# Kernel optimization log

Measured on AMD Instinct MI355X. Metric: run time of the kernel, lower is better.

The kernel has to match this reference:

```python
import jax, jax.numpy as jnp
import numpy as np

T, B, IN = 216, 16384, 8
H1, H2 = 16, 64


def _lstm_scan(xs, h0, c0, Wih, Whh, bih, bhh):
    # xs: [T, B, D_in]; returns all hidden states [T, B, H]
    def step(carry, x_t):
        h, c = carry
        g = x_t @ Wih.T + bih + h @ Whh.T + bhh  # [B, 4H]
        i, f, gg, o = jnp.split(g, 4, axis=-1)
        c = jax.nn.sigmoid(f) * c + jax.nn.sigmoid(i) * jnp.tanh(gg)
        h = jax.nn.sigmoid(o) * jnp.tanh(c)
        return (h, c), h
    (_, _), hs = jax.lax.scan(step, (h0, c0), xs)
    return hs


def setup_inputs() -> dict:
    key = jax.random.key(0)
    ks = jax.random.split(key, 24)
    def rn(k, shape, std):
        return jax.random.normal(k, shape, dtype=jnp.float32) * std
    # PyTorch LSTMCell/Linear default init: U(-1/sqrt(H), 1/sqrt(H)) -> use uniform
    def un(k, shape, bound):
        return jax.random.uniform(k, shape, dtype=jnp.float32, minval=-bound, maxval=bound)
    b1 = 1.0 / np.sqrt(H1)
    b2 = 1.0 / np.sqrt(H2)
    inp = {
        'x': jax.random.normal(ks[0], (T, B, IN), dtype=jnp.float32),
        # initial states: kaiming_normal_ with fan_in = last dim -> std = sqrt(2/fan_in)
        'h0f': rn(ks[1], (B, H1), np.sqrt(2.0 / H1)),
        'c0f': rn(ks[2], (B, H1), np.sqrt(2.0 / H1)),
        'h0b': rn(ks[3], (B, H1), np.sqrt(2.0 / H1)),
        'c0b': rn(ks[4], (B, H1), np.sqrt(2.0 / H1)),
        'h0m': rn(ks[5], (B, H2), np.sqrt(2.0 / H2)),
        'c0m': rn(ks[6], (B, H2), np.sqrt(2.0 / H2)),
        'Wih_f': un(ks[7], (4 * H1, IN), b1), 'Whh_f': un(ks[8], (4 * H1, H1), b1),
        'bih_f': un(ks[9], (4 * H1,), b1), 'bhh_f': un(ks[10], (4 * H1,), b1),
        'Wih_b': un(ks[11], (4 * H1, IN), b1), 'Whh_b': un(ks[12], (4 * H1, H1), b1),
        'bih_b': un(ks[13], (4 * H1,), b1), 'bhh_b': un(ks[14], (4 * H1,), b1),
        'Wih_m': un(ks[15], (4 * H2, 2 * H1), b2), 'Whh_m': un(ks[16], (4 * H2, H2), b2),
        'bih_m': un(ks[17], (4 * H2,), b2), 'bhh_m': un(ks[18], (4 * H2,), b2),
        'Wd': un(ks[19], (1, H2), b2), 'bd': un(ks[20], (1,), b2),
    }
    return inp


def reference(x, h0f, c0f, h0b, c0b, h0m, c0m,
              Wih_f, Whh_f, bih_f, bhh_f,
              Wih_b, Whh_b, bih_b, bhh_b,
              Wih_m, Whh_m, bih_m, bhh_m,
              Wd, bd):
    # forward direction LSTM over time
    hs_f = _lstm_scan(x, h0f, c0f, Wih_f, Whh_f, bih_f, bhh_f)          # [T,B,16]
    # backward direction: run on reversed sequence, then reverse outputs
    hs_b = _lstm_scan(x[::-1], h0b, c0b, Wih_b, Whh_b, bih_b, bhh_b)[::-1]  # [T,B,16]
    mid_in = jnp.concatenate([hs_f, hs_b], axis=-1)                     # [T,B,32]
    hs_m = _lstm_scan(mid_in, h0m, c0m, Wih_m, Whh_m, bih_m, bhh_m)     # [T,B,64]
    # dropout is identity in inference reference; dense 64->1 per step
    out = jnp.einsum('tbh,oh->tbo', hs_m, Wd) + bd                      # [T,B,1]
    return out[:, :, 0].T                                                # [B,T]
```

## Files before the change

kernel.cpp:

```cpp
#include <hip/hip_runtime.h>

#define TT 216
#define BB 16384
#define LOG2E 1.44269504088896340736f

typedef _Float16 h16;
typedef _Float16 half8 __attribute__((ext_vector_type(8)));
typedef float f32x4 __attribute__((ext_vector_type(4)));

__device__ __forceinline__ float rcp_f(float v) { return __builtin_amdgcn_rcpf(v); }
__device__ __forceinline__ float ex2(float v)   { return __builtin_amdgcn_exp2f(v); }

__device__ __forceinline__ float lstm_up(float pi, float pf, float pg, float po, float& cs)
{
    float ei = ex2(pi), ef = ex2(pf), eg = ex2(pg), eo = ex2(po);
    float Ei = 1.f + ei, Ef = 1.f + ef, Eg = 1.f + eg, Eo = 1.f + eo;
    float EiEg = Ei * Eg;
    float G = fmaf(2.f * LOG2E, Eg, -4.f * LOG2E);
    float N = fmaf(cs, EiEg, Ef * G);
    cs = N * rcp_f(Ef * EiEg);
    float pc = fminf(cs, 60.f);
    float Ec = 1.f + ex2(pc);
    return (Ec - 2.f) * rcp_f(Eo * Ec);
}

__global__ void prep_kernel(
    const float* __restrict__ Wih_f, const float* __restrict__ Whh_f,
    const float* __restrict__ bih_f, const float* __restrict__ bhh_f,
    const float* __restrict__ Wih_b, const float* __restrict__ Whh_b,
    const float* __restrict__ bih_b, const float* __restrict__ bhh_b,
    const float* __restrict__ Wih_m, const float* __restrict__ Whh_m,
    const float* __restrict__ bih_m, const float* __restrict__ bhh_m,
    h16* __restrict__ W1f, h16* __restrict__ W1b, h16* __restrict__ W2)
{
    int gtid = blockIdx.x * blockDim.x + threadIdx.x;
    int gs = gridDim.x * blockDim.x;
    for (int idx = gtid; idx < 64 * 32; idx += gs) {
        int n = idx >> 5, k = idx & 31;
        float a = ((n >> 4) == 2) ? 2.f * LOG2E : -LOG2E;
        float vf = 0.f, vb = 0.f;
        if (k < 8)        { vf = Wih_f[n * 8 + k];       vb = Wih_b[n * 8 + k]; }
        else if (k < 24)  { vf = Whh_f[n * 16 + k - 8];  vb = Whh_b[n * 16 + k - 8]; }
        else if (k == 24) { vf = bih_f[n] + bhh_f[n];    vb = bih_b[n] + bhh_b[n]; }
        W1f[idx] = (h16)(vf * a);
        W1b[idx] = (h16)(vb * a);
    }
    for (int idx = gtid; idx < 256 * 128; idx += gs) {
        int n = idx >> 7, k = idx & 127;
        float a = ((n >> 6) == 2) ? 2.f * LOG2E : -LOG2E;
        float v = 0.f;
        if (k < 32)       v = Wih_m[n * 32 + k];
        else if (k < 96)  v = Whh_m[n * 64 + k - 32];
        else if (k == 96) v = bih_m[n] + bhh_m[n];
        W2[idx] = (h16)(v * a);
    }
}

__global__ __launch_bounds__(256, 2) void small_lstm_kernel(
    const float* __restrict__ x,
    const float* __restrict__ h0f, const float* __restrict__ c0f,
    const float* __restrict__ h0b, const float* __restrict__ c0b,
    const h16* __restrict__ W1f, const h16* __restrict__ W1b,
    h16* __restrict__ hsf, h16* __restrict__ hsb)
{
    __shared__ __attribute__((aligned(16))) h16 hbuf[4][16][24];

    const int tid = threadIdx.x;
    const int wv = tid >> 6, lane = tid & 63;
    const int b = lane & 15, q = lane >> 4;

    const int wgid = blockIdx.x * 4 + wv;
    const int dir  = wgid & 1;
    const int base = (wgid >> 1) * 16;

    const float* h0 = dir ? h0b : h0f;
    const float* c0 = dir ? c0b : c0f;
    const h16* W1   = dir ? W1b : W1f;
    h16* hs = dir ? hsb : hsf;

    half8 bf0 = *(const half8*)(W1 + (0 * 16 + b) * 32 + q * 8);
    half8 bf1 = *(const half8*)(W1 + (1 * 16 + b) * 32 + q * 8);
    half8 bf2 = *(const half8*)(W1 + (2 * 16 + b) * 32 + q * 8);
    half8 bf3 = *(const half8*)(W1 + (3 * 16 + b) * 32 + q * 8);

    float cs0 = c0[(size_t)(base + q * 4 + 0) * 16 + b] * (2.f * LOG2E);
    float cs1 = c0[(size_t)(base + q * 4 + 1) * 16 + b] * (2.f * LOG2E);
    float cs2 = c0[(size_t)(base + q * 4 + 2) * 16 + b] * (2.f * LOG2E);
    float cs3 = c0[(size_t)(base + q * 4 + 3) * 16 + b] * (2.f * LOG2E);

    const int t0 = dir ? (TT - 1) : 0;

    half8 af;
    if (q == 0) {
        const float* xp = x + ((size_t)t0 * BB + base + b) * 8;
        f32x4 u0 = *(const f32x4*)xp, u1 = *(const f32x4*)(xp + 4);
        af[0] = (h16)u0[0]; af[1] = (h16)u0[1]; af[2] = (h16)u0[2]; af[3] = (h16)u0[3];
        af[4] = (h16)u1[0]; af[5] = (h16)u1[1]; af[6] = (h16)u1[2]; af[7] = (h16)u1[3];
    } else if (q == 3) {
        af[0] = (h16)1.f;
        af[1] = (h16)0.f; af[2] = (h16)0.f; af[3] = (h16)0.f;
        af[4] = (h16)0.f; af[5] = (h16)0.f; af[6] = (h16)0.f; af[7] = (h16)0.f;
    } else {
        const float* hp = h0 + (size_t)(base + b) * 16 + (q - 1) * 8;
        f32x4 u0 = *(const f32x4*)hp, u1 = *(const f32x4*)(hp + 4);
        af[0] = (h16)u0[0]; af[1] = (h16)u0[1]; af[2] = (h16)u0[2]; af[3] = (h16)u0[3];
        af[4] = (h16)u1[0]; af[5] = (h16)u1[1]; af[6] = (h16)u1[2]; af[7] = (h16)u1[3];
    }

    f32x4 xr[4][2];
    if (q == 0) {
#pragma unroll
        for (int u = 1; u <= 3; ++u) {
            int tl = dir ? (TT - 1 - u) : u;
            const float* xp = x + ((size_t)tl * BB + base + b) * 8;
            xr[u][0] = *(const f32x4*)xp;
            xr[u][1] = *(const f32x4*)(xp + 4);
        }
    }

    for (int it = 0; it < TT / 4; ++it) {
        half8 hst[4];
#pragma unroll
        for (int j = 0; j < 4; ++j) {
            const int s = it * 4 + j;

            f32x4 z0 = {0.f, 0.f, 0.f, 0.f}, z1 = z0, z2 = z0, z3 = z0;
            z0 = __builtin_amdgcn_mfma_f32_16x16x32_f16(af, bf0, z0, 0, 0, 0);
            z1 = __builtin_amdgcn_mfma_f32_16x16x32_f16(af, bf1, z1, 0, 0, 0);
            z2 = __builtin_amdgcn_mfma_f32_16x16x32_f16(af, bf2, z2, 0, 0, 0);
            z3 = __builtin_amdgcn_mfma_f32_16x16x32_f16(af, bf3, z3, 0, 0, 0);

            half8 xh;
            {
                const f32x4 u0 = xr[(j + 1) & 3][0], u1 = xr[(j + 1) & 3][1];
                xh[0] = (h16)u0[0]; xh[1] = (h16)u0[1]; xh[2] = (h16)u0[2]; xh[3] = (h16)u0[3];
                xh[4] = (h16)u1[0]; xh[5] = (h16)u1[1]; xh[6] = (h16)u1[2]; xh[7] = (h16)u1[3];
            }
            if (q == 0) {
                int ut = (s + 4 < TT) ? (s + 4) : (TT - 1);
                int tl = dir ? (TT - 1 - ut) : ut;
                const float* xp = x + ((size_t)tl * BB + base + b) * 8;
                xr[j][0] = *(const f32x4*)xp;
                xr[j][1] = *(const f32x4*)(xp + 4);
            }

            float hh0 = lstm_up(z0[0], z1[0], z2[0], z3[0], cs0);
            float hh1 = lstm_up(z0[1], z1[1], z2[1], z3[1], cs1);
            float hh2 = lstm_up(z0[2], z1[2], z2[2], z3[2], cs2);
            float hh3 = lstm_up(z0[3], z1[3], z2[3], z3[3], cs3);

            hbuf[wv][q * 4 + 0][b] = (h16)hh0;
            hbuf[wv][q * 4 + 1][b] = (h16)hh1;
            hbuf[wv][q * 4 + 2][b] = (h16)hh2;
            hbuf[wv][q * 4 + 3][b] = (h16)hh3;
            asm volatile("s_waitcnt lgkmcnt(0)" ::: "memory");
            half8 hv = *(const half8*)&hbuf[wv][b][(q == 2) ? 8 : 0];
            hst[j] = hv;

            if (q == 0)      af = xh;
            else if (q != 3) af = hv;
        }
        if (q == 1 || q == 2) {
#pragma unroll
            for (int j = 0; j < 4; ++j) {
                int s = it * 4 + j;
                int t = dir ? (TT - 1 - s) : s;
                *(half8*)(hs + ((size_t)t * BB + base + b) * 16 + (q - 1) * 8) = hst[j];
            }
        }
    }
}

__global__ __launch_bounds__(256, 4) void mid_lstm_kernel(
    const h16* __restrict__ hsf, const h16* __restrict__ hsb,
    const float* __restrict__ h0m, const float* __restrict__ c0m,
    const h16* __restrict__ W2,
    const float* __restrict__ Wd, const float* __restrict__ bdp,
    float* __restrict__ out)
{
    __shared__ __attribute__((aligned(16))) h16 Xs[2][16][104];
    __shared__ float outbuf[16][55];

    const int tid = threadIdx.x;
    const int base = blockIdx.x * 16;
    const int wv = tid >> 6, lane = tid & 63, col = lane & 15, q = lane >> 4;

    half8 bfr[4][3];
    float bp[4];
#pragma unroll
    for (int p = 0; p < 4; ++p) {
        int n = p * 64 + wv * 16 + col;
#pragma unroll
        for (int kt = 0; kt < 3; ++kt)
            bfr[p][kt] = *(const half8*)(W2 + (size_t)n * 128 + kt * 32 + q * 8);
        bp[p] = (float)W2[(size_t)n * 128 + 96];
    }
    half8 dfr[2];
#pragma unroll
    for (int kt = 0; kt < 2; ++kt)
#pragma unroll
        for (int j = 0; j < 8; ++j)
            dfr[kt][j] = (col == 0) ? (h16)Wd[kt * 32 + q * 8 + j] : (h16)0.f;
    const float bdv = bdp[0];

    float cs[4];
#pragma unroll
    for (int r = 0; r < 4; ++r)
        cs[r] = c0m[(size_t)(base + q * 4 + r) * 64 + wv * 16 + col] * (2.f * LOG2E);

    const h16* hsrc = (wv == 1) ? hsb : hsf;
    const int srow = lane >> 1, su8 = (lane & 1) * 8;
    if (wv < 2 && lane < 32) {
        uint4 v = *(const uint4*)(hsrc + ((size_t)0 * BB + base + srow) * 16 + su8);
        *(uint4*)&Xs[0][srow][wv * 16 + su8] = v;
    }
    {
        int row = tid >> 4, u4 = (tid & 15) * 4;
        float4 v = *(const float4*)(h0m + (size_t)(base + row) * 64 + u4);
        h16* d = &Xs[0][row][32 + u4];
        d[0] = (h16)v.x; d[1] = (h16)v.y; d[2] = (h16)v.z; d[3] = (h16)v.w;
    }
    uint4 ra, rb;
    if (wv < 2 && lane < 32) {
        ra = *(const uint4*)(hsrc + ((size_t)1 * BB + base + srow) * 16 + su8);
        rb = *(const uint4*)(hsrc + ((size_t)2 * BB + base + srow) * 16 + su8);
    }
    __syncthreads();

    for (int t = 0; t < TT; ++t) {
        const int cur = t & 1, nxt = cur ^ 1;
        if (wv < 2 && lane < 32) {
            if (t < TT - 1)
                *(uint4*)&Xs[nxt][srow][wv * 16 + su8] = ra;
            ra = rb;
            int tl = (t + 3 < TT) ? (t + 3) : (TT - 1);
            rb = *(const uint4*)(hsrc + ((size_t)tl * BB + base + srow) * 16 + su8);
        }
        half8 af[3];
#pragma unroll
        for (int kt = 0; kt < 3; ++kt)
            af[kt] = *(const half8*)&Xs[cur][col][kt * 32 + q * 8];
        if (wv == 3 && t > 0) {
            f32x4 z = {0.f, 0.f, 0.f, 0.f};
            z = __builtin_amdgcn_mfma_f32_16x16x32_f16(af[1], dfr[0], z, 0, 0, 0);
            z = __builtin_amdgcn_mfma_f32_16x16x32_f16(af[2], dfr[1], z, 0, 0, 0);
            if (col == 0) {
                int tc = (t - 1) % 54;
#pragma unroll
                for (int r = 0; r < 4; ++r)
                    outbuf[q * 4 + r][tc] = z[r] + bdv;
            }
        }
        f32x4 acc[4];
        __builtin_amdgcn_s_setprio(1);
#pragma unroll
        for (int p = 0; p < 4; ++p) {
            f32x4 z = {bp[p], bp[p], bp[p], bp[p]};
            z = __builtin_amdgcn_mfma_f32_16x16x32_f16(af[0], bfr[p][0], z, 0, 0, 0);
            z = __builtin_amdgcn_mfma_f32_16x16x32_f16(af[1], bfr[p][1], z, 0, 0, 0);
            z = __builtin_amdgcn_mfma_f32_16x16x32_f16(af[2], bfr[p][2], z, 0, 0, 0);
            acc[p] = z;
        }
        __builtin_amdgcn_s_setprio(0);
#pragma unroll
        for (int r = 0; r < 4; ++r) {
            float h = lstm_up(acc[0][r], acc[1][r], acc[2][r], acc[3][r], cs[r]);
            Xs[nxt][q * 4 + r][32 + wv * 16 + col] = (h16)h;
        }
        if (t > 0 && (t % 54) == 0) {
            __syncthreads();
            int off = t - 54;
            for (int idx = tid; idx < 16 * 54; idx += 256) {
                int row = idx / 54, cc = idx - row * 54;
                out[(size_t)(base + row) * TT + off + cc] = outbuf[row][cc];
            }
        }
        __syncthreads();
    }
    if (wv == 3) {
        half8 a1 = *(const half8*)&Xs[0][col][32 + q * 8];
        half8 a2 = *(const half8*)&Xs[0][col][64 + q * 8];
        f32x4 z = {0.f, 0.f, 0.f, 0.f};
        z = __builtin_amdgcn_mfma_f32_16x16x32_f16(a1, dfr[0], z, 0, 0, 0);
        z = __builtin_amdgcn_mfma_f32_16x16x32_f16(a2, dfr[1], z, 0, 0, 0);
        if (col == 0)
#pragma unroll
            for (int r = 0; r < 4; ++r)
                outbuf[q * 4 + r][53] = z[r] + bdv;
    }
    __syncthreads();
    for (int idx = tid; idx < 16 * 54; idx += 256) {
        int row = idx / 54, cc = idx - row * 54;
        out[(size_t)(base + row) * TT + 162 + cc] = outbuf[row][cc];
    }
}

extern "C" void kernel_launch(void* const* d_in, const int* in_sizes, int n_in,
                              void* d_out, int out_size, void* d_ws, size_t ws_size,
                              hipStream_t stream)
{
    const float* x     = (const float*)d_in[0];
    const float* h0f   = (const float*)d_in[1];
    const float* c0f   = (const float*)d_in[2];
    const float* h0b   = (const float*)d_in[3];
    const float* c0b   = (const float*)d_in[4];
    const float* h0m   = (const float*)d_in[5];
    const float* c0m   = (const float*)d_in[6];
    const float* Wih_f = (const float*)d_in[7];
    const float* Whh_f = (const float*)d_in[8];
    const float* bih_f = (const float*)d_in[9];
    const float* bhh_f = (const float*)d_in[10];
    const float* Wih_b = (const float*)d_in[11];
    const float* Whh_b = (const float*)d_in[12];
    const float* bih_b = (const float*)d_in[13];
    const float* bhh_b = (const float*)d_in[14];
    const float* Wih_m = (const float*)d_in[15];
    const float* Whh_m = (const float*)d_in[16];
    const float* bih_m = (const float*)d_in[17];
    const float* bhh_m = (const float*)d_in[18];
    const float* Wd    = (const float*)d_in[19];
    const float* bd    = (const float*)d_in[20];

    char* ws = (char*)d_ws;
    h16* W1f = (h16*)(ws + 0);
    h16* W1b = (h16*)(ws + 4096);
    h16* W2  = (h16*)(ws + 8192);
    h16* hsf = (h16*)(ws + 73728);
    h16* hsb = (h16*)(ws + 73728 + (size_t)TT * BB * 16 * 2);

    prep_kernel<<<64, 256, 0, stream>>>(Wih_f, Whh_f, bih_f, bhh_f,
                                        Wih_b, Whh_b, bih_b, bhh_b,
                                        Wih_m, Whh_m, bih_m, bhh_m,
                                        W1f, W1b, W2);
    small_lstm_kernel<<<512, 256, 0, stream>>>(x, h0f, c0f, h0b, c0b,
                                               W1f, W1b, hsf, hsb);
    mid_lstm_kernel<<<1024, 256, 0, stream>>>(hsf, hsb, h0m, c0m, W2,
                                              Wd, bd, (float*)d_out);
}
```

Measured before the change: 648.5 us.

## Process two independent 16-row batch tiles per block in mid LSTM kernel

The mid LSTM kernel now has each block handle 32 batch rows as two independent 16-row windows, so the grid is halved. Each wave interleaves two MFMA chains and two gate-update passes, which adds independent work to hide the latency of the serial recurrence. The per-step barrier and the recurrent weight fragments are now shared across twice the rows, and the input-staging and dense-output work is spread over more waves. In exchange register pressure roughly doubles, launch bounds drop to 2 blocks per CU, and the setprio hints are removed, so occupancy falls.

```diff
diff --git a/kernel.cpp b/kernel.cpp
--- a/kernel.cpp
+++ b/kernel.cpp
@@ -171,18 +171,18 @@
     }
 }
 
-__global__ __launch_bounds__(256, 4) void mid_lstm_kernel(
+__global__ __launch_bounds__(256, 2) void mid_lstm_kernel(
     const h16* __restrict__ hsf, const h16* __restrict__ hsb,
     const float* __restrict__ h0m, const float* __restrict__ c0m,
     const h16* __restrict__ W2,
     const float* __restrict__ Wd, const float* __restrict__ bdp,
     float* __restrict__ out)
 {
-    __shared__ __attribute__((aligned(16))) h16 Xs[2][16][104];
-    __shared__ float outbuf[16][55];
+    __shared__ __attribute__((aligned(16))) h16 Xs[2][2][16][104];
+    __shared__ float outbuf[2][16][55];
 
     const int tid = threadIdx.x;
-    const int base = blockIdx.x * 16;
+    const int base = blockIdx.x * 32;
     const int wv = tid >> 6, lane = tid & 63, col = lane & 15, q = lane >> 4;
 
     half8 bfr[4][3];
@@ -203,95 +203,122 @@
             dfr[kt][j] = (col == 0) ? (h16)Wd[kt * 32 + q * 8 + j] : (h16)0.f;
     const float bdv = bdp[0];
 
-    float cs[4];
-#pragma unroll
-    for (int r = 0; r < 4; ++r)
-        cs[r] = c0m[(size_t)(base + q * 4 + r) * 64 + wv * 16 + col] * (2.f * LOG2E);
-
-    const h16* hsrc = (wv == 1) ? hsb : hsf;
+    float csA[4], csB[4];
+#pragma unroll
+    for (int r = 0; r < 4; ++r) {
+        csA[r] = c0m[(size_t)(base + q * 4 + r) * 64 + wv * 16 + col] * (2.f * LOG2E);
+        csB[r] = c0m[(size_t)(base + 16 + q * 4 + r) * 64 + wv * 16 + col] * (2.f * LOG2E);
+    }
+
+    const h16* hsrc = (wv & 1) ? hsb : hsf;
+    const int mywin = wv >> 1;
     const int srow = lane >> 1, su8 = (lane & 1) * 8;
-    if (wv < 2 && lane < 32) {
-        uint4 v = *(const uint4*)(hsrc + ((size_t)0 * BB + base + srow) * 16 + su8);
-        *(uint4*)&Xs[0][srow][wv * 16 + su8] = v;
+    const int scol = (wv & 1) * 16 + su8;
+    const int grow = base + mywin * 16 + srow;
+
+    if (lane < 32) {
+        uint4 v = *(const uint4*)(hsrc + ((size_t)0 * BB + grow) * 16 + su8);
+        *(uint4*)&Xs[mywin][0][srow][scol] = v;
     }
     {
         int row = tid >> 4, u4 = (tid & 15) * 4;
-        float4 v = *(const float4*)(h0m + (size_t)(base + row) * 64 + u4);
-        h16* d = &Xs[0][row][32 + u4];
-        d[0] = (h16)v.x; d[1] = (h16)v.y; d[2] = (h16)v.z; d[3] = (h16)v.w;
+        float4 vA = *(const float4*)(h0m + (size_t)(base + row) * 64 + u4);
+        h16* dA = &Xs[0][0][row][32 + u4];
+        dA[0] = (h16)vA.x; dA[1] = (h16)vA.y; dA[2] = (h16)vA.z; dA[3] = (h16)vA.w;
+        float4 vB = *(const float4*)(h0m + (size_t)(base + 16 + row) * 64 + u4);
+        h16* dB = &Xs[1][0][row][32 + u4];
+        dB[0] = (h16)vB.x; dB[1] = (h16)vB.y; dB[2] = (h16)vB.z; dB[3] = (h16)vB.w;
     }
     uint4 ra, rb;
-    if (wv < 2 && lane < 32) {
-        ra = *(const uint4*)(hsrc + ((size_t)1 * BB + base + srow) * 16 + su8);
-        rb = *(const uint4*)(hsrc + ((size_t)2 * BB + base + srow) * 16 + su8);
+    if (lane < 32) {
+        ra = *(const uint4*)(hsrc + ((size_t)1 * BB + grow) * 16 + su8);
+        rb = *(const uint4*)(hsrc + ((size_t)2 * BB + grow) * 16 + su8);
     }
     __syncthreads();
 
     for (int t = 0; t < TT; ++t) {
         const int cur = t & 1, nxt = cur ^ 1;
-        if (wv < 2 && lane < 32) {
+        if (lane < 32) {
             if (t < TT - 1)
-                *(uint4*)&Xs[nxt][srow][wv * 16 + su8] = ra;
+                *(uint4*)&Xs[mywin][nxt][srow][scol] = ra;
             ra = rb;
             int tl = (t + 3 < TT) ? (t + 3) : (TT - 1);
-            rb = *(const uint4*)(hsrc + ((size_t)tl * BB + base + srow) * 16 + su8);
-        }
-        half8 af[3];
-#pragma unroll
-        for (int kt = 0; kt < 3; ++kt)
-            af[kt] = *(const half8*)&Xs[cur][col][kt * 32 + q * 8];
-        if (wv == 3 && t > 0) {
+            rb = *(const uint4*)(hsrc + ((size_t)tl * BB + grow) * 16 + su8);
+        }
+        half8 afA[3], afB[3];
+#pragma unroll
+        for (int kt = 0; kt < 3; ++kt) {
+            afA[kt] = *(const half8*)&Xs[0][cur][col][kt * 32 + q * 8];
+            afB[kt] = *(const half8*)&Xs[1][cur][col][kt * 32 + q * 8];
+        }
+        if ((wv & 1) && t > 0) {
+            half8 a1 = (wv == 1) ? afA[1] : afB[1];
+            half8 a2 = (wv == 1) ? afA[2] : afB[2];
             f32x4 z = {0.f, 0.f, 0.f, 0.f};
-            z = __builtin_amdgcn_mfma_f32_16x16x32_f16(af[1], dfr[0], z, 0, 0, 0);
-            z = __builtin_amdgcn_mfma_f32_16x16x32_f16(af[2], dfr[1], z, 0, 0, 0);
+            z = __builtin_amdgcn_mfma_f32_16x16x32_f16(a1, dfr[0], z, 0, 0, 0);
+            z = __builtin_amdgcn_mfma_f32_16x16x32_f16(a2, dfr[1], z, 0, 0, 0);
             if (col == 0) {
                 int tc = (t - 1) % 54;
 #pragma unroll
                 for (int r = 0; r < 4; ++r)
-                    outbuf[q * 4 + r][tc] = z[r] + bdv;
-            }
-        }
-        f32x4 acc[4];
-        __builtin_amdgcn_s_setprio(1);
+                    outbuf[wv >> 1][q * 4 + r][tc] = z[r] + bdv;
+            }
+        }
+        f32x4 accA[4], accB[4];
 #pragma unroll
         for (int p = 0; p < 4; ++p) {
             f32x4 z = {bp[p], bp[p], bp[p], bp[p]};
-            z = __builtin_amdgcn_mfma_f32_16x16x32_f16(af[0], bfr[p][0], z, 0, 0, 0);
-            z = __builtin_amdgcn_mfma_f32_16x16x32_f16(af[1], bfr[p][1], z, 0, 0, 0);
-            z = __builtin_amdgcn_mfma_f32_16x16x32_f16(af[2], bfr[p][2], z, 0, 0, 0);
-            acc[p] = z;
-        }
-        __builtin_amdgcn_s_setprio(0);
+            z = __builtin_amdgcn_mfma_f32_16x16x32_f16(afA[0], bfr[p][0], z, 0, 0, 0);
+            z = __builtin_amdgcn_mfma_f32_16x16x32_f16(afA[1], bfr[p][1], z, 0, 0, 0);
+            z = __builtin_amdgcn_mfma_f32_16x16x32_f16(afA[2], bfr[p][2], z, 0, 0, 0);
+            accA[p] = z;
+        }
+#pragma unroll
+        for (int p = 0; p < 4; ++p) {
+            f32x4 z = {bp[p], bp[p], bp[p], bp[p]};
+            z = __builtin_amdgcn_mfma_f32_16x16x32_f16(afB[0], bfr[p][0], z, 0, 0, 0);
+            z = __builtin_amdgcn_mfma_f32_16x16x32_f16(afB[1], bfr[p][1], z, 0, 0, 0);
+            z = __builtin_amdgcn_mfma_f32_16x16x32_f16(afB[2], bfr[p][2], z, 0, 0, 0);
+            accB[p] = z;
+        }
 #pragma unroll
         for (int r = 0; r < 4; ++r) {
-            float h = lstm_up(acc[0][r], acc[1][r], acc[2][r], acc[3][r], cs[r]);
-            Xs[nxt][q * 4 + r][32 + wv * 16 + col] = (h16)h;
+            float hA = lstm_up(accA[0][r], accA[1][r], accA[2][r], accA[3][r], csA[r]);
+            Xs[0][nxt][q * 4 + r][32 + wv * 16 + col] = (h16)hA;
+        }
+#pragma unroll
+        for (int r = 0; r < 4; ++r) {
+            float hB = lstm_up(accB[0][r], accB[1][r], accB[2][r], accB[3][r], csB[r]);
+            Xs[1][nxt][q * 4 + r][32 + wv * 16 + col] = (h16)hB;
         }
         if (t > 0 && (t % 54) == 0) {
             __syncthreads();
             int off = t - 54;
-            for (int idx = tid; idx < 16 * 54; idx += 256) {
-                int row = idx / 54, cc = idx - row * 54;
-                out[(size_t)(base + row) * TT + off + cc] = outbuf[row][cc];
+            for (int idx = tid; idx < 2 * 16 * 54; idx += 256) {
+                int w = idx / (16 * 54), rem = idx - w * 16 * 54;
+                int row = rem / 54, cc = rem - row * 54;
+                out[(size_t)(base + w * 16 + row) * TT + off + cc] = outbuf[w][row][cc];
             }
         }
         __syncthreads();
     }
-    if (wv == 3) {
-        half8 a1 = *(const half8*)&Xs[0][col][32 + q * 8];
-        half8 a2 = *(const half8*)&Xs[0][col][64 + q * 8];
+    if (wv & 1) {
+        const int w = wv >> 1;
+        half8 a1 = *(const half8*)&Xs[w][0][col][32 + q * 8];
+        half8 a2 = *(const half8*)&Xs[w][0][col][64 + q * 8];
         f32x4 z = {0.f, 0.f, 0.f, 0.f};
         z = __builtin_amdgcn_mfma_f32_16x16x32_f16(a1, dfr[0], z, 0, 0, 0);
         z = __builtin_amdgcn_mfma_f32_16x16x32_f16(a2, dfr[1], z, 0, 0, 0);
         if (col == 0)
 #pragma unroll
             for (int r = 0; r < 4; ++r)
-                outbuf[q * 4 + r][53] = z[r] + bdv;
+                outbuf[w][q * 4 + r][53] = z[r] + bdv;
     }
     __syncthreads();
-    for (int idx = tid; idx < 16 * 54; idx += 256) {
-        int row = idx / 54, cc = idx - row * 54;
-        out[(size_t)(base + row) * TT + 162 + cc] = outbuf[row][cc];
+    for (int idx = tid; idx < 2 * 16 * 54; idx += 256) {
+        int w = idx / (16 * 54), rem = idx - w * 16 * 54;
+        int row = rem / 54, cc = rem - row * 54;
+        out[(size_t)(base + w * 16 + row) * TT + 162 + cc] = outbuf[w][row][cc];
     }
 }
 
@@ -334,6 +361,6 @@
                                         W1f, W1b, W2);
     small_lstm_kernel<<<512, 256, 0, stream>>>(x, h0f, c0f, h0b, c0b,
                                                W1f, W1b, hsf, hsb);
-    mid_lstm_kernel<<<1024, 256, 0, stream>>>(hsf, hsb, h0m, c0m, W2,
-                                              Wd, bd, (float*)d_out);
-}
+    mid_lstm_kernel<<<512, 256, 0, stream>>>(hsf, hsb, h0m, c0m, W2,
+                                             Wd, bd, (float*)d_out);
+}
```

Measured after the change: 680.4 us. 4.9% more time.

## Transpose small-LSTM MFMA to keep hidden state in registers via ds_swizzle

Applied to the files above, without the earlier changes.

The small bidirectional LSTM kernel now swaps the MFMA operands so each lane's output holds four consecutive hidden units of one batch row. The hidden state is then passed on with a ds_swizzle exchange between lane groups instead of a round trip through shared memory and a wait. Hidden states are written straight to global memory each step as 8-byte stores instead of batched 16-byte stores. The mid kernel's s_setprio hints around its MFMA block are also removed. This targets per-step LDS latency on the serial recurrence, at the cost of smaller, more frequent global stores.

```diff
diff --git a/kernel.cpp b/kernel.cpp
--- a/kernel.cpp
+++ b/kernel.cpp
@@ -6,7 +6,10 @@
 
 typedef _Float16 h16;
 typedef _Float16 half8 __attribute__((ext_vector_type(8)));
+typedef _Float16 h4 __attribute__((ext_vector_type(4)));
 typedef float f32x4 __attribute__((ext_vector_type(4)));
+typedef int i2 __attribute__((ext_vector_type(2)));
+typedef int i4 __attribute__((ext_vector_type(4)));
 
 __device__ __forceinline__ float rcp_f(float v) { return __builtin_amdgcn_rcpf(v); }
 __device__ __forceinline__ float ex2(float v)   { return __builtin_amdgcn_exp2f(v); }
@@ -63,8 +66,6 @@
     const h16* __restrict__ W1f, const h16* __restrict__ W1b,
     h16* __restrict__ hsf, h16* __restrict__ hsb)
 {
-    __shared__ __attribute__((aligned(16))) h16 hbuf[4][16][24];
-
     const int tid = threadIdx.x;
     const int wv = tid >> 6, lane = tid & 63;
     const int b = lane & 15, q = lane >> 4;
@@ -78,33 +79,34 @@
     const h16* W1   = dir ? W1b : W1f;
     h16* hs = dir ? hsb : hsf;
 
-    half8 bf0 = *(const half8*)(W1 + (0 * 16 + b) * 32 + q * 8);
-    half8 bf1 = *(const half8*)(W1 + (1 * 16 + b) * 32 + q * 8);
-    half8 bf2 = *(const half8*)(W1 + (2 * 16 + b) * 32 + q * 8);
-    half8 bf3 = *(const half8*)(W1 + (3 * 16 + b) * 32 + q * 8);
-
-    float cs0 = c0[(size_t)(base + q * 4 + 0) * 16 + b] * (2.f * LOG2E);
-    float cs1 = c0[(size_t)(base + q * 4 + 1) * 16 + b] * (2.f * LOG2E);
-    float cs2 = c0[(size_t)(base + q * 4 + 2) * 16 + b] * (2.f * LOG2E);
-    float cs3 = c0[(size_t)(base + q * 4 + 3) * 16 + b] * (2.f * LOG2E);
+    half8 wf0 = *(const half8*)(W1 + (0 * 16 + b) * 32 + q * 8);
+    half8 wf1 = *(const half8*)(W1 + (1 * 16 + b) * 32 + q * 8);
+    half8 wf2 = *(const half8*)(W1 + (2 * 16 + b) * 32 + q * 8);
+    half8 wf3 = *(const half8*)(W1 + (3 * 16 + b) * 32 + q * 8);
+
+    f32x4 cv = *(const f32x4*)(c0 + (size_t)(base + b) * 16 + q * 4);
+    float cs0 = cv[0] * (2.f * LOG2E);
+    float cs1 = cv[1] * (2.f * LOG2E);
+    float cs2 = cv[2] * (2.f * LOG2E);
+    float cs3 = cv[3] * (2.f * LOG2E);
 
     const int t0 = dir ? (TT - 1) : 0;
 
-    half8 af;
+    half8 sf;
     if (q == 0) {
         const float* xp = x + ((size_t)t0 * BB + base + b) * 8;
         f32x4 u0 = *(const f32x4*)xp, u1 = *(const f32x4*)(xp + 4);
-        af[0] = (h16)u0[0]; af[1] = (h16)u0[1]; af[2] = (h16)u0[2]; af[3] = (h16)u0[3];
-        af[4] = (h16)u1[0]; af[5] = (h16)u1[1]; af[6] = (h16)u1[2]; af[7] = (h16)u1[3];
+        sf[0] = (h16)u0[0]; sf[1] = (h16)u0[1]; sf[2] = (h16)u0[2]; sf[3] = (h16)u0[3];
+        sf[4] = (h16)u1[0]; sf[5] = (h16)u1[1]; sf[6] = (h16)u1[2]; sf[7] = (h16)u1[3];
     } else if (q == 3) {
-        af[0] = (h16)1.f;
-        af[1] = (h16)0.f; af[2] = (h16)0.f; af[3] = (h16)0.f;
-        af[4] = (h16)0.f; af[5] = (h16)0.f; af[6] = (h16)0.f; af[7] = (h16)0.f;
+        sf[0] = (h16)1.f;
+        sf[1] = (h16)0.f; sf[2] = (h16)0.f; sf[3] = (h16)0.f;
+        sf[4] = (h16)0.f; sf[5] = (h16)0.f; sf[6] = (h16)0.f; sf[7] = (h16)0.f;
     } else {
         const float* hp = h0 + (size_t)(base + b) * 16 + (q - 1) * 8;
         f32x4 u0 = *(const f32x4*)hp, u1 = *(const f32x4*)(hp + 4);
-        af[0] = (h16)u0[0]; af[1] = (h16)u0[1]; af[2] = (h16)u0[2]; af[3] = (h16)u0[3];
-        af[4] = (h16)u1[0]; af[5] = (h16)u1[1]; af[6] = (h16)u1[2]; af[7] = (h16)u1[3];
+        sf[0] = (h16)u0[0]; sf[1] = (h16)u0[1]; sf[2] = (h16)u0[2]; sf[3] = (h16)u0[3];
+        sf[4] = (h16)u1[0]; sf[5] = (h16)u1[1]; sf[6] = (h16)u1[2]; sf[7] = (h16)u1[3];
     }
 
     f32x4 xr[4][2];
@@ -119,16 +121,16 @@
     }
 
     for (int it = 0; it < TT / 4; ++it) {
-        half8 hst[4];
 #pragma unroll
         for (int j = 0; j < 4; ++j) {
             const int s = it * 4 + j;
+            const int t = dir ? (TT - 1 - s) : s;
 
             f32x4 z0 = {0.f, 0.f, 0.f, 0.f}, z1 = z0, z2 = z0, z3 = z0;
-            z0 = __builtin_amdgcn_mfma_f32_16x16x32_f16(af, bf0, z0, 0, 0, 0);
-            z1 = __builtin_amdgcn_mfma_f32_16x16x32_f16(af, bf1, z1, 0, 0, 0);
-            z2 = __builtin_amdgcn_mfma_f32_16x16x32_f16(af, bf2, z2, 0, 0, 0);
-            z3 = __builtin_amdgcn_mfma_f32_16x16x32_f16(af, bf3, z3, 0, 0, 0);
+            z0 = __builtin_amdgcn_mfma_f32_16x16x32_f16(wf0, sf, z0, 0, 0, 0);
+            z1 = __builtin_amdgcn_mfma_f32_16x16x32_f16(wf1, sf, z1, 0, 0, 0);
+            z2 = __builtin_amdgcn_mfma_f32_16x16x32_f16(wf2, sf, z2, 0, 0, 0);
+            z3 = __builtin_amdgcn_mfma_f32_16x16x32_f16(wf3, sf, z3, 0, 0, 0);
 
             half8 xh;
             {
@@ -149,24 +151,23 @@
             float hh2 = lstm_up(z0[2], z1[2], z2[2], z3[2], cs2);
             float hh3 = lstm_up(z0[3], z1[3], z2[3], z3[3], cs3);
 
-            hbuf[wv][q * 4 + 0][b] = (h16)hh0;
-            hbuf[wv][q * 4 + 1][b] = (h16)hh1;
-            hbuf[wv][q * 4 + 2][b] = (h16)hh2;
-            hbuf[wv][q * 4 + 3][b] = (h16)hh3;
-            asm volatile("s_waitcnt lgkmcnt(0)" ::: "memory");
-            half8 hv = *(const half8*)&hbuf[wv][b][(q == 2) ? 8 : 0];
-            hst[j] = hv;
-
-            if (q == 0)      af = xh;
-            else if (q != 3) af = hv;
-        }
-        if (q == 1 || q == 2) {
-#pragma unroll
-            for (int j = 0; j < 4; ++j) {
-                int s = it * 4 + j;
-                int t = dir ? (TT - 1 - s) : s;
-                *(half8*)(hs + ((size_t)t * BB + base + b) * 16 + (q - 1) * 8) = hst[j];
-            }
+            h4 hv;
+            hv[0] = (h16)hh0; hv[1] = (h16)hh1; hv[2] = (h16)hh2; hv[3] = (h16)hh3;
+            *(h4*)(hs + ((size_t)t * BB + base + b) * 16 + q * 4) = hv;
+
+            i2 pk = __builtin_bit_cast(i2, hv);
+            int sp0 = __builtin_amdgcn_ds_swizzle(pk[0], 0x401F);
+            int sp1 = __builtin_amdgcn_ds_swizzle(pk[1], 0x401F);
+
+            i4 nw;
+            nw[0] = (q == 1) ? sp0 : pk[0];
+            nw[1] = (q == 1) ? sp1 : pk[1];
+            nw[2] = (q == 1) ? pk[0] : sp0;
+            nw[3] = (q == 1) ? pk[1] : sp1;
+            half8 nf = __builtin_bit_cast(half8, nw);
+
+            if (q == 0)      sf = xh;
+            else if (q != 3) sf = nf;
         }
     }
 }
@@ -252,7 +253,6 @@
             }
         }
         f32x4 acc[4];
-        __builtin_amdgcn_s_setprio(1);
 #pragma unroll
         for (int p = 0; p < 4; ++p) {
             f32x4 z = {bp[p], bp[p], bp[p], bp[p]};
@@ -261,7 +261,6 @@
             z = __builtin_amdgcn_mfma_f32_16x16x32_f16(af[2], bfr[p][2], z, 0, 0, 0);
             acc[p] = z;
         }
-        __builtin_amdgcn_s_setprio(0);
 #pragma unroll
         for (int r = 0; r < 4; ++r) {
             float h = lstm_up(acc[0][r], acc[1][r], acc[2][r], acc[3][r], cs[r]);
```

Measured after the change: 609.1 us. -6.1%, faster.
